# Kernel optimization log

Measured on AMD Instinct MI355X. Metric: run time of the kernel, lower is better.

## Reference

```python
import jax, jax.numpy as jnp
import numpy as np

# Mamba defaults for d_model=128: expand=2 -> d_inner=256, d_state=16,
# dt_rank=ceil(128/16)=8, d_conv=4. Six directional scans (NDIR=6).
D_MODEL = 128; D_INNER = 256; D_STATE = 16; DT_RANK = 8; D_CONV = 4; NDIR = 6
B_SZ = 2; VD = 16; VH = 16; VW = 16  # volume dims -> L = 4096


def setup_inputs() -> dict:
    key = jax.random.key(0)
    ks = jax.random.split(key, 8)
    s = 0.05
    return {
        "input": jax.random.normal(ks[0], (B_SZ, D_MODEL, VD, VH, VW), jnp.float32),
        "W_in": jax.random.normal(ks[1], (NDIR, 2 * D_INNER, D_MODEL), jnp.float32) * s,
        "conv_w": jax.random.normal(ks[2], (NDIR, D_INNER, D_CONV), jnp.float32) * s,
        "conv_b": jnp.zeros((NDIR, D_INNER), jnp.float32),
        "W_xproj": jax.random.normal(ks[3], (NDIR, DT_RANK + 2 * D_STATE, D_INNER), jnp.float32) * s,
        "W_dt": jax.random.normal(ks[4], (NDIR, D_INNER, DT_RANK), jnp.float32) * s,
        "b_dt": jax.random.normal(ks[5], (NDIR, D_INNER), jnp.float32) * s - 4.0,  # softplus(-4)~0.018, mamba-like dt init
        "A_log": jnp.log(jnp.broadcast_to(jnp.arange(1, D_STATE + 1, dtype=jnp.float32), (NDIR, D_INNER, D_STATE)) + 0.0),
        "Dparam": jnp.ones((NDIR, D_INNER), jnp.float32),
        "W_out": jax.random.normal(ks[6], (NDIR, D_MODEL, D_INNER), jnp.float32) * s,
    }


def _mamba(x, W_in, conv_w, conv_b, W_xproj, W_dt, b_dt, A_log, Dparam, W_out):
    # x: (B, L, d_model) -> (B, L, d_model). Faithful to mamba_ssm defaults (no in/out proj bias).
    Bsz, L, _ = x.shape
    xz = jnp.einsum('bld,ed->ble', x, W_in)          # (B, L, 2*d_inner)
    xc, z = jnp.split(xz, 2, axis=-1)
    d_inner = xc.shape[-1]
    # causal depthwise conv1d (left pad d_conv-1, truncate to L == mamba's pad+slice)
    xt = xc.transpose(0, 2, 1)                       # (B, d_inner, L)
    k = conv_w[:, None, :]                           # (d_inner, 1, d_conv)
    xt = jax.lax.conv_general_dilated(xt, k, (1,), [(D_CONV - 1, 0)],
                                      dimension_numbers=('NCH', 'OIH', 'NCH'),
                                      feature_group_count=d_inner)
    xc = jax.nn.silu((xt + conv_b[None, :, None]).transpose(0, 2, 1))  # (B, L, d_inner)
    x_dbl = jnp.einsum('bld,ed->ble', xc, W_xproj)   # (B, L, dt_rank + 2*d_state)
    dt, Bs, Cs = jnp.split(x_dbl, [DT_RANK, DT_RANK + D_STATE], axis=-1)
    dt = jax.nn.softplus(jnp.einsum('blr,dr->bld', dt, W_dt) + b_dt)   # (B, L, d_inner)
    A = -jnp.exp(A_log)                              # (d_inner, d_state)

    def step(h, inp):
        dt_t, B_t, C_t, x_t = inp                    # (B,di), (B,ds), (B,ds), (B,di)
        dA = jnp.exp(dt_t[..., None] * A)            # (B, di, ds)
        h = dA * h + (dt_t * x_t)[..., None] * B_t[:, None, :]
        y = jnp.einsum('bdn,bn->bd', h, C_t)
        return h, y

    h0 = jnp.zeros((Bsz, d_inner, D_STATE), xc.dtype)
    _, ys = jax.lax.scan(step, h0, (dt.transpose(1, 0, 2), Bs.transpose(1, 0, 2),
                                    Cs.transpose(1, 0, 2), xc.transpose(1, 0, 2)))
    y = ys.transpose(1, 0, 2) + xc * Dparam          # (B, L, d_inner)
    y = y * jax.nn.silu(z)
    return jnp.einsum('bld,ed->ble', y, W_out)       # (B, L, d_model)


def reference(input, W_in, conv_w, conv_b, W_xproj, W_dt, b_dt, A_log, Dparam, W_out):
    Bsz, C, D, H, W = input.shape
    x1 = input.reshape(Bsz, C, -1).transpose(0, 2, 1)                                  # (B, L, C)
    x2 = jnp.swapaxes(input, 3, 4).reshape(Bsz, C, -1).transpose(0, 2, 1)
    x3 = jnp.rot90(input, 1, axes=(2, 4)).reshape(Bsz, C, -1).transpose(0, 2, 1)
    xs = jnp.stack([x1, x2, x3, jnp.flip(x1, 1), jnp.flip(x2, 1), jnp.flip(x3, 1)])    # (6, B, L, C)
    ys = jax.vmap(_mamba)(xs, W_in, conv_w, conv_b, W_xproj, W_dt, b_dt, A_log, Dparam, W_out)
    y1 = ys[0].transpose(0, 2, 1).reshape(Bsz, C, -1)
    y2 = ys[1].transpose(0, 2, 1).reshape(Bsz, C, D, W, H).swapaxes(3, 4).reshape(Bsz, C, -1)
    y3 = jnp.rot90(ys[2].transpose(0, 2, 1).reshape(Bsz, C, W, H, D), -1, axes=(2, 4)).reshape(Bsz, C, -1)
    y4 = jnp.flip(ys[3].transpose(0, 2, 1), 2).reshape(Bsz, C, -1)
    y5 = jnp.flip(ys[4].transpose(0, 2, 1), 2).reshape(Bsz, C, D, W, H).swapaxes(3, 4).reshape(Bsz, C, -1)
    y6 = jnp.rot90(jnp.flip(ys[5].transpose(0, 2, 1), 2).reshape(Bsz, C, W, H, D), -1, axes=(2, 4)).reshape(Bsz, C, -1)
    return (y1 + y2 + y3 + y4 + y5 + y6) / 6.0
```

## Files before the change

### kernel.cpp

```cpp
#include <hip/hip_runtime.h>
#include <cmath>

#define LOG2E 1.44269504088896340736f
#define LN2F  0.69314718055994530942f

__device__ __forceinline__ int perm_l_to_s(int dir, int l) {
    int m = (dir >= 3) ? (4095 - l) : l;
    int r = (dir >= 3) ? (dir - 3) : dir;
    if (r == 0) return m;
    if (r == 1) return (m & 0xF00) | ((m & 0x00F) << 4) | ((m >> 4) & 0xF);
    return ((m & 0x00F) << 8) | (m & 0x0F0) | (15 - (m >> 8));
}

__device__ __forceinline__ float silu_f(float v) {
    return v / (1.f + __expf(-v));
}

__device__ __forceinline__ float softplus_f(float s) {
    return fmaxf(s, 0.f) + LN2F * __log2f(1.f + __expf(-fabsf(s)));
}

__global__ __launch_bounds__(256) void k_prep(const float* __restrict__ W_in,
                                              const float* __restrict__ W_out,
                                              float* __restrict__ WinT,
                                              float* __restrict__ WoutT) {
    int idx = blockIdx.x * 256 + threadIdx.x;
    if (idx < 393216) {
        int dir = idx >> 16;
        int r = idx & 65535;
        int c = r >> 9;
        int e = r & 511;
        WinT[idx] = W_in[dir * 65536 + e * 128 + c];
    } else if (idx < 393216 + 196608) {
        int j = idx - 393216;
        int k = j >> 7;
        int cc = j & 127;
        int dir = k >> 8;
        int d = k & 255;
        WoutT[j] = W_out[dir * 32768 + cc * 256 + d];
    }
}

__global__ __launch_bounds__(256) void k_gemm_in(const float* __restrict__ in,
                                                 const float* __restrict__ WinT,
                                                 float* __restrict__ xbuf,
                                                 float* __restrict__ zbuf,
                                                 int dirBase) {
    __shared__ float As[32][132];
    __shared__ float Bs[32][132];
    const int tid = threadIdx.x;
    const int dirg = blockIdx.z;
    const int dir = dirBase + dirg;
    const int m0 = blockIdx.x * 128;
    const int n0 = blockIdx.y * 128;
    const int b = m0 >> 12;
    const int l0 = m0 & 4095;
    const float* Wd = WinT + dir * 65536;
    float acc[8][8] = {};
    const int tx = tid & 15, ty = tid >> 4;
    const int lm = tid & 127, lk = tid >> 7;
    const int sA = perm_l_to_s(dir, l0 + lm);
    const size_t abase = ((size_t)b << 19) + (size_t)sA;
    #pragma unroll 1
    for (int k0 = 0; k0 < 128; k0 += 32) {
        #pragma unroll
        for (int i = 0; i < 16; ++i) {
            int kk = lk + i * 2;
            As[kk][lm] = in[abase + ((size_t)(k0 + kk) << 12)];
            Bs[kk][lm] = Wd[(k0 + kk) * 512 + n0 + lm];
        }
        __syncthreads();
        #pragma unroll
        for (int kk = 0; kk < 32; ++kk) {
            float a[8], bb[8];
            *(float4*)&a[0]  = *(const float4*)&As[kk][ty * 8];
            *(float4*)&a[4]  = *(const float4*)&As[kk][ty * 8 + 4];
            *(float4*)&bb[0] = *(const float4*)&Bs[kk][tx * 4];
            *(float4*)&bb[4] = *(const float4*)&Bs[kk][64 + tx * 4];
            #pragma unroll
            for (int i = 0; i < 8; ++i)
                #pragma unroll
                for (int j = 0; j < 8; ++j)
                    acc[i][j] = fmaf(a[i], bb[j], acc[i][j]);
        }
        __syncthreads();
    }
    const int gz = dirg * 2 + b;
    float* dst = (n0 < 256) ? xbuf : zbuf;
    const int ecl = (n0 + tx * 4) & 255;
    const int ech = (n0 + 64 + tx * 4) & 255;
    #pragma unroll
    for (int i = 0; i < 8; ++i) {
        int l = l0 + ty * 8 + i;
        size_t rowo = ((size_t)gz * 4096 + l) * 256;
        *(float4*)&dst[rowo + ecl] = make_float4(acc[i][0], acc[i][1], acc[i][2], acc[i][3]);
        *(float4*)&dst[rowo + ech] = make_float4(acc[i][4], acc[i][5], acc[i][6], acc[i][7]);
    }
}

__global__ __launch_bounds__(256) void k_convxproj(const float* __restrict__ xbuf,
                                                   const float* __restrict__ cw,
                                                   const float* __restrict__ cb,
                                                   const float* __restrict__ Wxp,
                                                   const float* __restrict__ Wdt,
                                                   const float* __restrict__ bdt,
                                                   float2* __restrict__ dxp,
                                                   float* __restrict__ BC,
                                                   int dirBase) {
    __shared__ float xs[16][260];
    __shared__ float xd[16][44];
    const int tid = threadIdx.x;
    const int gz = blockIdx.y;
    const int dir = dirBase + (gz >> 1);
    const int bl0 = blockIdx.x * 16;
    const int d = tid;
    const float* xb = xbuf + (size_t)gz * 4096 * 256;
    {
        float xv[19];
        #pragma unroll
        for (int r = 0; r < 19; ++r) {
            int row = bl0 - 3 + r;
            xv[r] = (row >= 0) ? xb[(size_t)row * 256 + d] : 0.f;
        }
        float4 w = *(const float4*)&cw[dir * 1024 + d * 4];
        float cbv = cb[dir * 256 + d];
        #pragma unroll
        for (int lr = 0; lr < 16; ++lr) {
            float a = cbv;
            a = fmaf(w.x, xv[lr], a);
            a = fmaf(w.y, xv[lr + 1], a);
            a = fmaf(w.z, xv[lr + 2], a);
            a = fmaf(w.w, xv[lr + 3], a);
            xs[lr][d] = silu_f(a);
        }
    }
    __syncthreads();
    const float* Wp = Wxp + dir * 10240;
    {
        const int lr = tid & 15, rq = tid >> 4;
        const float4* xrow = (const float4*)&xs[lr][0];
        const float4* w0 = (const float4*)(Wp + rq * 256);
        const float4* w1 = (const float4*)(Wp + (rq + 16) * 256);
        const float4* w2 = (const float4*)(Wp + ((rq < 8) ? (rq + 32) : rq) * 256);
        float s0a = 0.f, s0b = 0.f, s1a = 0.f, s1b = 0.f, s2a = 0.f, s2b = 0.f;
        #pragma unroll 8
        for (int q = 0; q < 64; q += 2) {
            float4 x0 = xrow[q], x1 = xrow[q + 1];
            float4 a0 = w0[q], a1 = w0[q + 1];
            s0a = fmaf(x0.x, a0.x, s0a); s0a = fmaf(x0.y, a0.y, s0a);
            s0a = fmaf(x0.z, a0.z, s0a); s0a = fmaf(x0.w, a0.w, s0a);
            s0b = fmaf(x1.x, a1.x, s0b); s0b = fmaf(x1.y, a1.y, s0b);
            s0b = fmaf(x1.z, a1.z, s0b); s0b = fmaf(x1.w, a1.w, s0b);
            float4 b0 = w1[q], b1 = w1[q + 1];
            s1a = fmaf(x0.x, b0.x, s1a); s1a = fmaf(x0.y, b0.y, s1a);
            s1a = fmaf(x0.z, b0.z, s1a); s1a = fmaf(x0.w, b0.w, s1a);
            s1b = fmaf(x1.x, b1.x, s1b); s1b = fmaf(x1.y, b1.y, s1b);
            s1b = fmaf(x1.z, b1.z, s1b); s1b = fmaf(x1.w, b1.w, s1b);
            float4 c0 = w2[q], c1 = w2[q + 1];
            s2a = fmaf(x0.x, c0.x, s2a); s2a = fmaf(x0.y, c0.y, s2a);
            s2a = fmaf(x0.z, c0.z, s2a); s2a = fmaf(x0.w, c0.w, s2a);
            s2b = fmaf(x1.x, c1.x, s2b); s2b = fmaf(x1.y, c1.y, s2b);
            s2b = fmaf(x1.z, c1.z, s2b); s2b = fmaf(x1.w, c1.w, s2b);
        }
        xd[lr][rq] = s0a + s0b;
        xd[lr][rq + 16] = s1a + s1b;
        if (rq < 8) xd[lr][rq + 32] = s2a + s2b;
    }
    __syncthreads();
    {
        float4 wa = *(const float4*)&Wdt[dir * 2048 + d * 8];
        float4 wb = *(const float4*)&Wdt[dir * 2048 + d * 8 + 4];
        float bb = bdt[dir * 256 + d];
        #pragma unroll 4
        for (int lr = 0; lr < 16; ++lr) {
            float4 xda = *(const float4*)&xd[lr][0];
            float4 xdb = *(const float4*)&xd[lr][4];
            float s = bb;
            s = fmaf(xda.x, wa.x, s); s = fmaf(xda.y, wa.y, s);
            s = fmaf(xda.z, wa.z, s); s = fmaf(xda.w, wa.w, s);
            s = fmaf(xdb.x, wb.x, s); s = fmaf(xdb.y, wb.y, s);
            s = fmaf(xdb.z, wb.z, s); s = fmaf(xdb.w, wb.w, s);
            float sp = softplus_f(s);
            dxp[((size_t)gz * 4096 + bl0 + lr) * 256 + d] = make_float2(sp, xs[lr][d]);
        }
    }
    for (int t2 = tid; t2 < 512; t2 += 256) {
        int lr = t2 >> 5, n = t2 & 31;
        BC[((size_t)gz * 4096 + bl0 + lr) * 32 + n] = xd[lr][8 + n];
    }
}

__device__ __forceinline__ void pow_ladder(float E, int nh, float* dA) {
    float E2 = E * E, E4 = E2 * E2, E8 = E4 * E4;
    float base = nh ? E8 : 1.f;
    dA[0] = base * E;
    dA[1] = base * E2;
    dA[2] = dA[0] * E2;
    dA[3] = base * E4;
    dA[4] = dA[0] * E4;
    dA[5] = dA[1] * E4;
    dA[6] = dA[2] * E4;
    dA[7] = base * E8;
}

__global__ __launch_bounds__(256) void k_scan1(const float2* __restrict__ dxp,
                                               const float* __restrict__ BC,
                                               float* __restrict__ P,
                                               float* __restrict__ hend) {
    const int tid = threadIdx.x;
    const int ln = tid & 63, w = tid >> 6;
    const int dq = ln & 31, nh = ln >> 5;
    const int d = blockIdx.x * 128 + w * 32 + dq;
    const int c = blockIdx.y;
    const int gz = blockIdx.z;
    float h[8] = {0.f,0.f,0.f,0.f,0.f,0.f,0.f,0.f};
    float sdt = 0.f;
    const int R0 = gz * 4096 + c * 64;
    #pragma unroll 4
    for (int t = 0; t < 64; ++t) {
        int R = R0 + t;
        float2 dx = dxp[(size_t)R * 256 + d];
        float4 b0 = *(const float4*)&BC[(size_t)R * 32 + nh * 8];
        float4 b1 = *(const float4*)&BC[(size_t)R * 32 + nh * 8 + 4];
        float E = __expf(-dx.x);
        float dA[8];
        pow_ladder(E, nh, dA);
        float du = dx.x * dx.y;
        float Bv[8] = {b0.x, b0.y, b0.z, b0.w, b1.x, b1.y, b1.z, b1.w};
        #pragma unroll
        for (int j = 0; j < 8; ++j)
            h[j] = fmaf(dA[j], h[j], du * Bv[j]);
        sdt += dx.x;
    }
    float Es = __expf(-sdt);
    float q[8];
    pow_ladder(Es, nh, q);
    int o = (gz * 64 + c) * 4096 + d * 16 + nh * 8;
    *(float4*)&P[o]        = make_float4(q[0], q[1], q[2], q[3]);
    *(float4*)&P[o + 4]    = make_float4(q[4], q[5], q[6], q[7]);
    *(float4*)&hend[o]     = make_float4(h[0], h[1], h[2], h[3]);
    *(float4*)&hend[o + 4] = make_float4(h[4], h[5], h[6], h[7]);
}

__global__ __launch_bounds__(256) void k_scan2(const float* __restrict__ P,
                                               const float* __restrict__ hend,
                                               float* __restrict__ Sbuf) {
    const int gz = blockIdx.y;
    const int dn = blockIdx.x * 256 + threadIdx.x;
    float s = 0.f;
    for (int c = 0; c < 64; ++c) {
        int o = (gz * 64 + c) * 4096 + dn;
        Sbuf[o] = s;
        s = fmaf(P[o], s, hend[o]);
    }
}

__global__ __launch_bounds__(256) void k_scan3(const float2* __restrict__ dxp,
                                               const float* __restrict__ BC,
                                               const float* __restrict__ zbuf,
                                               const float* __restrict__ Dp,
                                               const float* __restrict__ Sbuf,
                                               float* __restrict__ y,
                                               int ystr, int dirBase) {
    const int tid = threadIdx.x;
    const int ln = tid & 63, w = tid >> 6;
    const int dq = ln & 31, nh = ln >> 5;
    const int d = blockIdx.x * 128 + w * 32 + dq;
    const int c = blockIdx.y;
    const int gz = blockIdx.z;
    const int dir = dirBase + (gz >> 1);
    const int b = gz & 1;
    const int koff = (ystr == 1536) ? dir * 256 : 0;
    const float Dpv = Dp[dir * 256 + d];
    int o = (gz * 64 + c) * 4096 + d * 16 + nh * 8;
    float4 s0 = *(const float4*)&Sbuf[o];
    float4 s1 = *(const float4*)&Sbuf[o + 4];
    float h[8] = {s0.x, s0.y, s0.z, s0.w, s1.x, s1.y, s1.z, s1.w};
    const int R0 = gz * 4096 + c * 64;
    #pragma unroll 4
    for (int t = 0; t < 64; ++t) {
        int R = R0 + t;
        float2 dx = dxp[(size_t)R * 256 + d];
        float4 b0 = *(const float4*)&BC[(size_t)R * 32 + nh * 8];
        float4 b1 = *(const float4*)&BC[(size_t)R * 32 + nh * 8 + 4];
        float4 c0 = *(const float4*)&BC[(size_t)R * 32 + 16 + nh * 8];
        float4 c1 = *(const float4*)&BC[(size_t)R * 32 + 16 + nh * 8 + 4];
        float E = __expf(-dx.x);
        float dA[8];
        pow_ladder(E, nh, dA);
        float du = dx.x * dx.y;
        float Bv[8] = {b0.x, b0.y, b0.z, b0.w, b1.x, b1.y, b1.z, b1.w};
        float Cv[8] = {c0.x, c0.y, c0.z, c0.w, c1.x, c1.y, c1.z, c1.w};
        float yv = 0.f;
        #pragma unroll
        for (int j = 0; j < 8; ++j) {
            h[j] = fmaf(dA[j], h[j], du * Bv[j]);
            yv = fmaf(h[j], Cv[j], yv);
        }
        yv += __shfl_xor(yv, 32);
        if (nh == 0) {
            float zv = zbuf[(size_t)R * 256 + d];
            float g = zv / (1.f + __expf(-zv));
            float outv = fmaf(dx.y, Dpv, yv) * g;
            int l = c * 64 + t;
            int s = perm_l_to_s(dir, l);
            y[(size_t)(b * 4096 + s) * ystr + koff + d] = outv;
        }
    }
}

__global__ __launch_bounds__(256) void k_gemm_out_split(const float* __restrict__ y,
                                                        const float* __restrict__ W,
                                                        float* __restrict__ pp,
                                                        int kt) {
    __shared__ float As[32][132];
    __shared__ float Bs[32][132];
    const int tid = threadIdx.x;
    const int m0 = blockIdx.x * 128;
    const int kz = blockIdx.z;
    const int kb = kz * kt;
    const int tx = tid & 15, ty = tid >> 4;
    float acc[8][8] = {};
    #pragma unroll 1
    for (int k0 = 0; k0 < kt; k0 += 32) {
        #pragma unroll
        for (int i = 0; i < 4; ++i) {
            int idx = tid + 256 * i;
            int kf = idx & 7, mloc = idx >> 3;
            float4 v = *(const float4*)&y[(size_t)(m0 + mloc) * 1536 + kb + k0 + kf * 4];
            As[kf * 4 + 0][mloc] = v.x;
            As[kf * 4 + 1][mloc] = v.y;
            As[kf * 4 + 2][mloc] = v.z;
            As[kf * 4 + 3][mloc] = v.w;
        }
        #pragma unroll
        for (int i = 0; i < 4; ++i) {
            int idx = tid + 256 * i;
            int kk = idx >> 5, nq = idx & 31;
            float4 v = *(const float4*)&W[(size_t)(kb + k0 + kk) * 128 + nq * 4];
            *(float4*)&Bs[kk][nq * 4] = v;
        }
        __syncthreads();
        #pragma unroll
        for (int kk = 0; kk < 32; ++kk) {
            float a[8], bb[8];
            *(float4*)&a[0]  = *(const float4*)&As[kk][ty * 8];
            *(float4*)&a[4]  = *(const float4*)&As[kk][ty * 8 + 4];
            *(float4*)&bb[0] = *(const float4*)&Bs[kk][tx * 4];
            *(float4*)&bb[4] = *(const float4*)&Bs[kk][64 + tx * 4];
            #pragma unroll
            for (int i = 0; i < 8; ++i)
                #pragma unroll
                for (int j = 0; j < 8; ++j)
                    acc[i][j] = fmaf(a[i], bb[j], acc[i][j]);
        }
        __syncthreads();
    }
    const int b = m0 >> 12;
    const int s0 = (m0 & 4095) + ty * 8;
    #pragma unroll
    for (int j = 0; j < 4; ++j) {
        int ccl = tx * 4 + j;
        size_t o = ((size_t)(kz * 2 + b) * 128 + ccl) * 4096 + s0;
        *(float4*)&pp[o]     = make_float4(acc[0][j], acc[1][j], acc[2][j], acc[3][j]);
        *(float4*)&pp[o + 4] = make_float4(acc[4][j], acc[5][j], acc[6][j], acc[7][j]);
        int cch = 64 + tx * 4 + j;
        o = ((size_t)(kz * 2 + b) * 128 + cch) * 4096 + s0;
        *(float4*)&pp[o]     = make_float4(acc[0][4 + j], acc[1][4 + j], acc[2][4 + j], acc[3][4 + j]);
        *(float4*)&pp[o + 4] = make_float4(acc[4][4 + j], acc[5][4 + j], acc[6][4 + j], acc[7][4 + j]);
    }
}

__global__ __launch_bounds__(256) void k_redout(const float4* __restrict__ pp,
                                                float4* __restrict__ out, int KS) {
    int t = blockIdx.x * 256 + threadIdx.x;
    float4 s = pp[t];
    for (int k = 1; k < KS; ++k) {
        float4 v = pp[(size_t)k * 262144 + t];
        s.x += v.x; s.y += v.y; s.z += v.z; s.w += v.w;
    }
    const float sc = 1.f / 6.f;
    out[t] = make_float4(s.x * sc, s.y * sc, s.z * sc, s.w * sc);
}

__global__ __launch_bounds__(256) void k_gemm_out_acc(const float* __restrict__ A,
                                                      const float* __restrict__ W,
                                                      float* __restrict__ out) {
    __shared__ float As[64][34];
    __shared__ float Bs[64][64];
    const int tid = threadIdx.x;
    const int m0 = blockIdx.x * 32;
    const int n0 = blockIdx.y * 64;
    const int tx = tid & 15, ty = tid >> 4;
    const int mr = tid >> 3, kq = tid & 7;
    const int lm = tid & 63, lk = tid >> 6;
    float acc[2][4] = {{0.f,0.f,0.f,0.f},{0.f,0.f,0.f,0.f}};
    for (int k0 = 0; k0 < 256; k0 += 64) {
        #pragma unroll
        for (int ksub = 0; ksub < 2; ++ksub) {
            int koffl = (ksub * 8 + kq) * 4;
            float4 v = *(const float4*)&A[(size_t)(m0 + mr) * 256 + k0 + koffl];
            As[koffl + 0][mr] = v.x;
            As[koffl + 1][mr] = v.y;
            As[koffl + 2][mr] = v.z;
            As[koffl + 3][mr] = v.w;
        }
        #pragma unroll
        for (int i = 0; i < 16; ++i) {
            int kk = lk + i * 4;
            Bs[kk][lm] = W[(k0 + kk) * 128 + n0 + lm];
        }
        __syncthreads();
        #pragma unroll 8
        for (int kk = 0; kk < 64; ++kk) {
            float2 av = *(const float2*)&As[kk][ty * 2];
            float4 bv = *(const float4*)&Bs[kk][tx * 4];
            acc[0][0] = fmaf(av.x, bv.x, acc[0][0]);
            acc[0][1] = fmaf(av.x, bv.y, acc[0][1]);
            acc[0][2] = fmaf(av.x, bv.z, acc[0][2]);
            acc[0][3] = fmaf(av.x, bv.w, acc[0][3]);
            acc[1][0] = fmaf(av.y, bv.x, acc[1][0]);
            acc[1][1] = fmaf(av.y, bv.y, acc[1][1]);
            acc[1][2] = fmaf(av.y, bv.z, acc[1][2]);
            acc[1][3] = fmaf(av.y, bv.w, acc[1][3]);
        }
        __syncthreads();
    }
    const float sc = 1.f / 6.f;
    #pragma unroll
    for (int i = 0; i < 2; ++i) {
        int mm = m0 + ty * 2 + i;
        int b = mm >> 12, s = mm & 4095;
        #pragma unroll
        for (int j = 0; j < 4; ++j) {
            size_t o = (size_t)b * 524288 + (size_t)(n0 + tx * 4 + j) * 4096 + s;
            out[o] += acc[i][j] * sc;
        }
    }
}

extern "C" void kernel_launch(void* const* d_in, const int* in_sizes, int n_in,
                              void* d_out, int out_size, void* d_ws, size_t ws_size,
                              hipStream_t stream) {
    (void)in_sizes; (void)n_in;
    const float* input   = (const float*)d_in[0];
    const float* W_in    = (const float*)d_in[1];
    const float* conv_w  = (const float*)d_in[2];
    const float* conv_b  = (const float*)d_in[3];
    const float* W_xproj = (const float*)d_in[4];
    const float* W_dt    = (const float*)d_in[5];
    const float* b_dt    = (const float*)d_in[6];
    const float* Dparam  = (const float*)d_in[8];
    const float* W_out   = (const float*)d_in[9];
    float* out = (float*)d_out;
    float* ws = (float*)d_ws;

    const long fixed  = 589824;
    const long perdir = 10223616;
    const long y1536  = 12582912;
    const size_t wsf = ws_size / 4;

    int G; int lite = 0;
    if      (wsf >= (size_t)(fixed + 6 * perdir))          G = 6;
    else if (wsf >= (size_t)(fixed + 3 * perdir + y1536))  G = 3;
    else if (wsf >= (size_t)(fixed + 2 * perdir + y1536))  G = 2;
    else if (wsf >= (size_t)(fixed + 1 * perdir + y1536))  G = 1;
    else { G = 1; lite = 1; }

    float* WinT  = ws;
    float* WoutT = ws + 393216;
    float* p = ws + fixed;
    float* BC   = p; p += (long)G * 262144;
    float* P    = p; p += (long)G * 524288;
    float* hend = p; p += (long)G * 524288;
    float* Sbuf = p; p += (long)G * 524288;
    float* zbuf = p; p += (long)G * 2097152;
    float2* dxp = (float2*)p; p += (long)G * 4194304;
    float* xbuf = p; p += (long)G * 2097152;
    float* y;
    int ystr;
    if (lite)        { y = p; ystr = 256; }
    else if (G == 6) { y = xbuf; ystr = 1536; }
    else             { y = p; ystr = 1536; }
    int KS = (G >= 3) ? 4 : (G == 2 ? 2 : 1);
    float* pp = P;

    k_prep<<<2304, 256, 0, stream>>>(W_in, W_out, WinT, WoutT);

    if (!lite) {
        for (int g = 0; g < 6; g += G) {
            k_gemm_in<<<dim3(64, 4, G), 256, 0, stream>>>(input, WinT, xbuf, zbuf, g);
            k_convxproj<<<dim3(256, 2 * G), 256, 0, stream>>>(xbuf, conv_w, conv_b,
                                                              W_xproj, W_dt, b_dt,
                                                              dxp, BC, g);
            k_scan1<<<dim3(2, 64, 2 * G), 256, 0, stream>>>(dxp, BC, P, hend);
            k_scan2<<<dim3(16, 2 * G), 256, 0, stream>>>(P, hend, Sbuf);
            k_scan3<<<dim3(2, 64, 2 * G), 256, 0, stream>>>(dxp, BC, zbuf,
                                                            Dparam, Sbuf, y, 1536, g);
        }
        k_gemm_out_split<<<dim3(64, 1, KS), 256, 0, stream>>>(y, WoutT, pp, 1536 / KS);
        k_redout<<<1024, 256, 0, stream>>>((const float4*)pp, (float4*)out, KS);
    } else {
        hipMemsetAsync(d_out, 0, (size_t)out_size * sizeof(float), stream);
        for (int dir = 0; dir < 6; ++dir) {
            k_gemm_in<<<dim3(64, 4, 1), 256, 0, stream>>>(input, WinT, xbuf, zbuf, dir);
            k_convxproj<<<dim3(256, 2), 256, 0, stream>>>(xbuf, conv_w, conv_b,
                                                          W_xproj, W_dt, b_dt,
                                                          dxp, BC, dir);
            k_scan1<<<dim3(2, 64, 2), 256, 0, stream>>>(dxp, BC, P, hend);
            k_scan2<<<dim3(16, 2), 256, 0, stream>>>(P, hend, Sbuf);
            k_scan3<<<dim3(2, 64, 2), 256, 0, stream>>>(dxp, BC, zbuf,
                                                        Dparam, Sbuf, y, 256, dir);
            k_gemm_out_acc<<<dim3(256, 2), 256, 0, stream>>>(y, WoutT + dir * 256 * 128, out);
        }
    }
}
```

Baseline: 412.9 us.

## Pre-transpose permuted inputs for coalesced gemm_in loads and atomically accumulate out-projection

Adds a pre-pass that materializes the swapped and rotated input layouts, so the input GEMM reads contiguous addresses instead of gathering through the scan permutation. It also replaces the split-K out-projection's partial buffer and separate reduction kernel with atomicAdd directly into a zeroed output. This removes one kernel launch and a partial-sum round trip through memory. In exchange it adds an extra transpose pass, repeated inside each direction group, plus scalar atomics that may contend and make float summation order nondeterministic.

```diff
diff --git a/kernel.cpp b/kernel.cpp
--- a/kernel.cpp
+++ b/kernel.cpp
@@ -41,11 +41,25 @@
     }
 }
 
+__global__ __launch_bounds__(256) void k_pretrans(const float* __restrict__ in,
+                                                  float* __restrict__ inS,
+                                                  float* __restrict__ inR) {
+    int idx = blockIdx.x * 256 + threadIdx.x;
+    int s = idx & 4095;
+    int base = idx & ~4095;
+    int ss = (s & 0xF00) | ((s & 0x00F) << 4) | ((s >> 4) & 0xF);
+    int sr = ((s & 0x00F) << 8) | (s & 0x0F0) | (15 - (s >> 8));
+    inS[idx] = in[base + ss];
+    inR[idx] = in[base + sr];
+}
+
 __global__ __launch_bounds__(256) void k_gemm_in(const float* __restrict__ in,
+                                                 const float* __restrict__ inS,
+                                                 const float* __restrict__ inR,
                                                  const float* __restrict__ WinT,
                                                  float* __restrict__ xbuf,
                                                  float* __restrict__ zbuf,
-                                                 int dirBase) {
+                                                 int dirBase, int pre) {
     __shared__ float As[32][132];
     __shared__ float Bs[32][132];
     const int tid = threadIdx.x;
@@ -59,14 +73,23 @@
     float acc[8][8] = {};
     const int tx = tid & 15, ty = tid >> 4;
     const int lm = tid & 127, lk = tid >> 7;
-    const int sA = perm_l_to_s(dir, l0 + lm);
+    int sA;
+    const float* Ab;
+    if (pre) {
+        int r = (dir >= 3) ? dir - 3 : dir;
+        Ab = (r == 0) ? in : (r == 1) ? inS : inR;
+        sA = (dir >= 3) ? (4095 - (l0 + lm)) : (l0 + lm);
+    } else {
+        Ab = in;
+        sA = perm_l_to_s(dir, l0 + lm);
+    }
     const size_t abase = ((size_t)b << 19) + (size_t)sA;
     #pragma unroll 1
     for (int k0 = 0; k0 < 128; k0 += 32) {
         #pragma unroll
         for (int i = 0; i < 16; ++i) {
             int kk = lk + i * 2;
-            As[kk][lm] = in[abase + ((size_t)(k0 + kk) << 12)];
+            As[kk][lm] = Ab[abase + ((size_t)(k0 + kk) << 12)];
             Bs[kk][lm] = Wd[(k0 + kk) * 512 + n0 + lm];
         }
         __syncthreads();
@@ -309,10 +332,10 @@
     }
 }
 
-__global__ __launch_bounds__(256) void k_gemm_out_split(const float* __restrict__ y,
-                                                        const float* __restrict__ W,
-                                                        float* __restrict__ pp,
-                                                        int kt) {
+__global__ __launch_bounds__(256) void k_gemm_out_atomic(const float* __restrict__ y,
+                                                         const float* __restrict__ W,
+                                                         float* __restrict__ out,
+                                                         int kt) {
     __shared__ float As[32][132];
     __shared__ float Bs[32][132];
     const int tid = threadIdx.x;
@@ -356,31 +379,17 @@
         }
         __syncthreads();
     }
+    const float sc = 1.f / 6.f;
     const int b = m0 >> 12;
     const int s0 = (m0 & 4095) + ty * 8;
     #pragma unroll
-    for (int j = 0; j < 4; ++j) {
-        int ccl = tx * 4 + j;
-        size_t o = ((size_t)(kz * 2 + b) * 128 + ccl) * 4096 + s0;
-        *(float4*)&pp[o]     = make_float4(acc[0][j], acc[1][j], acc[2][j], acc[3][j]);
-        *(float4*)&pp[o + 4] = make_float4(acc[4][j], acc[5][j], acc[6][j], acc[7][j]);
-        int cch = 64 + tx * 4 + j;
-        o = ((size_t)(kz * 2 + b) * 128 + cch) * 4096 + s0;
-        *(float4*)&pp[o]     = make_float4(acc[0][4 + j], acc[1][4 + j], acc[2][4 + j], acc[3][4 + j]);
-        *(float4*)&pp[o + 4] = make_float4(acc[4][4 + j], acc[5][4 + j], acc[6][4 + j], acc[7][4 + j]);
-    }
-}
-
-__global__ __launch_bounds__(256) void k_redout(const float4* __restrict__ pp,
-                                                float4* __restrict__ out, int KS) {
-    int t = blockIdx.x * 256 + threadIdx.x;
-    float4 s = pp[t];
-    for (int k = 1; k < KS; ++k) {
-        float4 v = pp[(size_t)k * 262144 + t];
-        s.x += v.x; s.y += v.y; s.z += v.z; s.w += v.w;
-    }
-    const float sc = 1.f / 6.f;
-    out[t] = make_float4(s.x * sc, s.y * sc, s.z * sc, s.w * sc);
+    for (int j = 0; j < 8; ++j) {
+        int cc = (j < 4) ? (tx * 4 + j) : (64 + tx * 4 + (j - 4));
+        size_t o = (size_t)b * 524288 + (size_t)cc * 4096 + s0;
+        #pragma unroll
+        for (int i = 0; i < 8; ++i)
+            atomicAdd(&out[o + i], acc[i][j] * sc);
+    }
 }
 
 __global__ __launch_bounds__(256) void k_gemm_out_acc(const float* __restrict__ A,
@@ -482,14 +491,20 @@
     if (lite)        { y = p; ystr = 256; }
     else if (G == 6) { y = xbuf; ystr = 1536; }
     else             { y = p; ystr = 1536; }
-    int KS = (G >= 3) ? 4 : (G == 2 ? 2 : 1);
-    float* pp = P;
+    int pre = (!lite && G >= 2) ? 1 : 0;
+    float* inS = P;
+    float* inR = P + 1048576;
+    int KS = 4;
 
     k_prep<<<2304, 256, 0, stream>>>(W_in, W_out, WinT, WoutT);
 
     if (!lite) {
+        hipMemsetAsync(d_out, 0, (size_t)out_size * sizeof(float), stream);
         for (int g = 0; g < 6; g += G) {
-            k_gemm_in<<<dim3(64, 4, G), 256, 0, stream>>>(input, WinT, xbuf, zbuf, g);
+            if (pre)
+                k_pretrans<<<4096, 256, 0, stream>>>(input, inS, inR);
+            k_gemm_in<<<dim3(64, 4, G), 256, 0, stream>>>(input, inS, inR, WinT,
+                                                          xbuf, zbuf, g, pre);
             k_convxproj<<<dim3(256, 2 * G), 256, 0, stream>>>(xbuf, conv_w, conv_b,
                                                               W_xproj, W_dt, b_dt,
                                                               dxp, BC, g);
@@ -498,12 +513,12 @@
             k_scan3<<<dim3(2, 64, 2 * G), 256, 0, stream>>>(dxp, BC, zbuf,
                                                             Dparam, Sbuf, y, 1536, g);
         }
-        k_gemm_out_split<<<dim3(64, 1, KS), 256, 0, stream>>>(y, WoutT, pp, 1536 / KS);
-        k_redout<<<1024, 256, 0, stream>>>((const float4*)pp, (float4*)out, KS);
+        k_gemm_out_atomic<<<dim3(64, 1, KS), 256, 0, stream>>>(y, WoutT, out, 1536 / KS);
     } else {
         hipMemsetAsync(d_out, 0, (size_t)out_size * sizeof(float), stream);
         for (int dir = 0; dir < 6; ++dir) {
-            k_gemm_in<<<dim3(64, 4, 1), 256, 0, stream>>>(input, WinT, xbuf, zbuf, dir);
+            k_gemm_in<<<dim3(64, 4, 1), 256, 0, stream>>>(input, input, input, WinT,
+                                                          xbuf, zbuf, dir, 0);
             k_convxproj<<<dim3(256, 2), 256, 0, stream>>>(xbuf, conv_w, conv_b,
                                                           W_xproj, W_dt, b_dt,
                                                           dxp, BC, dir);
```

New measurement: 509.8 us. 1.23x slower.
